# Optimization experiments

Measured on AMD Instinct MI355X. Metric: run time of the kernel, lower is better.

## Reference

```python
import jax, jax.numpy as jnp
import numpy as np

B, T, S, H = 4, 256, 512, 512


def setup_inputs() -> dict:
    key = jax.random.key(0)
    ks = jax.random.split(key, 8)
    scale = 1.0 / np.sqrt(H)
    return {
        "decoder_hidden": jax.random.normal(ks[0], (B, T, H), jnp.float32),
        "encoder_outputs": jax.random.normal(ks[1], (B, S, H), jnp.float32),
        "W1": jax.random.uniform(ks[2], (H, H), jnp.float32, -scale, scale),
        "b1": jax.random.uniform(ks[3], (H,), jnp.float32, -scale, scale),
        "W2": jax.random.uniform(ks[4], (H, H), jnp.float32, -scale, scale),
        "b2": jax.random.uniform(ks[5], (H,), jnp.float32, -scale, scale),
        "V": jax.random.uniform(ks[6], (H,), jnp.float32, -scale, scale),
        "bV": jax.random.uniform(ks[7], (), jnp.float32, -scale, scale),
    }


def reference(decoder_hidden, encoder_outputs, W1, b1, W2, b2, V, bV):
    # Projections: q (B,T,H), k (B,S,H)
    q = jnp.einsum("bth,hd->btd", decoder_hidden, W1.T) + b1
    k = jnp.einsum("bsh,hd->bsd", encoder_outputs, W2.T) + b2
    # Additive scores: tanh over broadcast (B,T,S,H), reduced by V -> (B,T,S)
    e = jnp.tanh(q[:, :, None, :] + k[:, None, :, :])
    score = jnp.einsum("btsh,h->bts", e, V) + bV
    attn = jax.nn.softmax(score, axis=-1)
    # Context: (B,T,S) @ (B,S,H) -> (B,T,H)
    context = jnp.einsum("bts,bsh->bth", attn, encoder_outputs)
    return context
```

## Files before the change

kernel.cpp:

```cpp
#include <hip/hip_runtime.h>

#define B 4
#define T 256
#define S 512
#define H 512
#define BT (B*T)

#define PRESCALE 2.8853900817779268f
#define LOG2E 1.4426950408889634f
#define QCLAMP 15.0f

typedef unsigned short u16;
typedef __attribute__((ext_vector_type(8))) short bf16x8;
typedef __attribute__((ext_vector_type(4))) float f32x4;

#if __has_builtin(__builtin_amdgcn_exp2f)
#define EXP2(x) __builtin_amdgcn_exp2f(x)
#else
#define EXP2(x) exp2f(x)
#endif

__device__ __forceinline__ u16 f2bf(float x) {
    unsigned u = __float_as_uint(x);
    u = u + 0x7FFFu + ((u >> 16) & 1u);
    return (u16)(u >> 16);
}

__device__ __forceinline__ void split8(float4 f0, float4 f1, bf16x8& hi, bf16x8& lo) {
    float x[8] = {f0.x, f0.y, f0.z, f0.w, f1.x, f1.y, f1.z, f1.w};
    #pragma unroll
    for (int i = 0; i < 8; ++i) {
        unsigned u = __float_as_uint(x[i]);
        unsigned h = u & 0xFFFF0000u;
        hi[i] = (short)(h >> 16);
        lo[i] = (short)f2bf(x[i] - __uint_as_float(h));
    }
}

__global__ __launch_bounds__(256) void mfma_proj(
    const float* __restrict__ dh, const float* __restrict__ enc,
    const float* __restrict__ W1, const float* __restrict__ W2,
    const float* __restrict__ b1, const float* __restrict__ b2,
    float* __restrict__ abuf, float* __restrict__ bT4,
    u16* __restrict__ encT_hi, u16* __restrict__ encT_lo)
{
    __shared__ u16 lds[4 * 4096];

    const int tid   = threadIdx.x;
    const int n0    = blockIdx.x * 64;
    const int mTile = blockIdx.y;

    if (mTile >= 48) {
        float (*TTf)[65] = reinterpret_cast<float(*)[65]>(lds);
        const int ty = mTile - 48;
        const int bb = ty >> 3;
        const int st = ty & 7;
        const int c64 = tid & 63;
        const int r4  = tid >> 6;
        #pragma unroll
        for (int rr = 0; rr < 16; ++rr) {
            const int r = rr * 4 + r4;
            TTf[r][c64] = enc[((size_t)(bb * S + st * 64 + r)) * H + n0 + c64];
        }
        __syncthreads();
        const int hr = tid >> 2;
        const int sq = (tid & 3) * 16;
        u16* ehp = encT_hi + ((size_t)(bb * H + n0 + hr)) * S + st * 64 + sq;
        u16* elp = encT_lo + ((size_t)(bb * H + n0 + hr)) * S + st * 64 + sq;
        #pragma unroll
        for (int j4 = 0; j4 < 4; ++j4) {
            ushort4 hv, lv;
            #pragma unroll
            for (int jj = 0; jj < 4; ++jj) {
                float x = TTf[sq + j4 * 4 + jj][hr];
                unsigned u = __float_as_uint(x);
                unsigned hb = u & 0xFFFF0000u;
                u16 hh = (u16)(hb >> 16);
                u16 ll = f2bf(x - __uint_as_float(hb));
                if (jj == 0) { hv.x = hh; lv.x = ll; }
                else if (jj == 1) { hv.y = hh; lv.y = ll; }
                else if (jj == 2) { hv.z = hh; lv.z = ll; }
                else { hv.w = hh; lv.w = ll; }
            }
            *(ushort4*)&ehp[j4 * 4] = hv;
            *(ushort4*)&elp[j4 * 4] = lv;
        }
        return;
    }

    const int lane  = tid & 63;
    const int w     = tid >> 6;
    const int mbase = mTile * 64;
    const bool is_q = (mTile < 16);

    const float* Asrc = is_q ? dh : enc;
    const float* Wsrc = is_q ? W1 : W2;
    const int arow = is_q ? mbase : (mbase - 1024);

    const int wm = (w & 1) * 32;
    const int wn = (w >> 1) * 32;

    const int r0  = tid >> 3;
    const int kc0 = tid & 7;

    f32x4 acc[2][2] = {};

    for (int kb = 0; kb < 8; ++kb) {
        const int k0 = kb * 64 + kc0 * 8;
        const size_t ga0 = (size_t)(arow + r0) * 512 + k0;
        const size_t ga1 = (size_t)(arow + r0 + 32) * 512 + k0;
        const size_t gw0 = (size_t)(n0 + r0) * 512 + k0;
        const size_t gw1 = (size_t)(n0 + r0 + 32) * 512 + k0;
        bf16x8 ah0, al0, ah1, al1, wh0, wl0, wh1, wl1;
        split8(*(const float4*)&Asrc[ga0], *(const float4*)&Asrc[ga0 + 4], ah0, al0);
        split8(*(const float4*)&Asrc[ga1], *(const float4*)&Asrc[ga1 + 4], ah1, al1);
        split8(*(const float4*)&Wsrc[gw0], *(const float4*)&Wsrc[gw0 + 4], wh0, wl0);
        split8(*(const float4*)&Wsrc[gw1], *(const float4*)&Wsrc[gw1 + 4], wh1, wl1);
        __syncthreads();
        const int sw  = (kc0 ^ (r0 & 7)) << 3;
        const int s0o = r0 * 64 + sw;
        const int s1o = (r0 + 32) * 64 + sw;
        *(bf16x8*)&lds[0 * 4096 + s0o] = ah0;  *(bf16x8*)&lds[0 * 4096 + s1o] = ah1;
        *(bf16x8*)&lds[1 * 4096 + s0o] = al0;  *(bf16x8*)&lds[1 * 4096 + s1o] = al1;
        *(bf16x8*)&lds[2 * 4096 + s0o] = wh0;  *(bf16x8*)&lds[2 * 4096 + s1o] = wh1;
        *(bf16x8*)&lds[3 * 4096 + s0o] = wl0;  *(bf16x8*)&lds[3 * 4096 + s1o] = wl1;
        __syncthreads();

        #pragma unroll
        for (int ks = 0; ks < 2; ++ks) {
            const int kg = ks * 4 + (lane >> 4);
            bf16x8 amh[2], aml[2], bnh[2], bnl[2];
            #pragma unroll
            for (int ms = 0; ms < 2; ++ms) {
                const int row = wm + ms * 16 + (lane & 15);
                const int off = row * 64 + ((kg ^ (row & 7)) << 3);
                amh[ms] = *(const bf16x8*)&lds[0 * 4096 + off];
                aml[ms] = *(const bf16x8*)&lds[1 * 4096 + off];
            }
            #pragma unroll
            for (int ns = 0; ns < 2; ++ns) {
                const int row = wn + ns * 16 + (lane & 15);
                const int off = row * 64 + ((kg ^ (row & 7)) << 3);
                bnh[ns] = *(const bf16x8*)&lds[2 * 4096 + off];
                bnl[ns] = *(const bf16x8*)&lds[3 * 4096 + off];
            }
            #pragma unroll
            for (int ms = 0; ms < 2; ++ms)
                #pragma unroll
                for (int ns = 0; ns < 2; ++ns) {
                    acc[ms][ns] = __builtin_amdgcn_mfma_f32_16x16x32_bf16(amh[ms], bnh[ns], acc[ms][ns], 0, 0, 0);
                    acc[ms][ns] = __builtin_amdgcn_mfma_f32_16x16x32_bf16(amh[ms], bnl[ns], acc[ms][ns], 0, 0, 0);
                    acc[ms][ns] = __builtin_amdgcn_mfma_f32_16x16x32_bf16(aml[ms], bnh[ns], acc[ms][ns], 0, 0, 0);
                }
        }
    }

    const float* bias = is_q ? b1 : b2;
    #pragma unroll
    for (int ns = 0; ns < 2; ++ns) {
        const int gn = n0 + wn + ns * 16 + (lane & 15);
        const float bv = bias[gn];
        #pragma unroll
        for (int ms = 0; ms < 2; ++ms) {
            #pragma unroll
            for (int r = 0; r < 4; ++r) {
                const int gm = mbase + wm + ms * 16 + (lane >> 4) * 4 + r;
                const float e = EXP2(fminf((acc[ms][ns][r] + bv) * PRESCALE, QCLAMP));
                if (is_q) {
                    abuf[(size_t)gm * 512 + gn] = e;
                } else {
                    const int srow = gm - 1024;
                    const int bb = srow >> 9, ss = srow & 511;
                    bT4[(((size_t)(bb * 128 + (gn >> 2)) * 512) + ss) * 4 + (gn & 3)] = e;
                }
            }
        }
    }
}

__device__ __forceinline__ float quad_term(float4 qa, float4 kb, float4 v4, float acc) {
    float x0 = fmaf(qa.x, kb.x, 1.f);
    float x1 = fmaf(qa.y, kb.y, 1.f);
    float x2 = fmaf(qa.z, kb.z, 1.f);
    float x3 = fmaf(qa.w, kb.w, 1.f);
    float p01 = x0 * x1, p23 = x2 * x3;
    float n01 = fmaf(v4.y, x0, v4.x * x1);
    float n23 = fmaf(v4.w, x2, v4.z * x3);
    float num = fmaf(n23, p01, n01 * p23);
    float den = p01 * p23;
    return fmaf(num, __builtin_amdgcn_rcpf(den), acc);
}

__global__ __launch_bounds__(512) void score_e(
    const float* __restrict__ abuf, const float* __restrict__ bT4,
    const float* __restrict__ Vp, const float* __restrict__ bVp,
    u16* __restrict__ e_hi, u16* __restrict__ e_lo, float* __restrict__ Zp)
{
    const int tid  = threadIdx.x;
    const int lane = tid & 63;
    const int w    = tid >> 6;
    const int sc   = blockIdx.x;
    const int t0   = blockIdx.y * 16;
    const int b    = blockIdx.z;
    const int s0   = sc * 64;

    float pv = 0.f;
    #pragma unroll
    for (int i = 0; i < 8; ++i) pv += Vp[i * 64 + lane];
    #pragma unroll
    for (int off = 32; off; off >>= 1) pv += __shfl_xor(pv, off);
    pv += bVp[0];

    const int ta = t0 + w * 2;
    const int tb = ta + 1;
    const float* aA = abuf + __builtin_amdgcn_readfirstlane((b * T + ta) * H);
    const float* aB = abuf + __builtin_amdgcn_readfirstlane((b * T + tb) * H);
    const float4* bp = (const float4*)bT4 + (size_t)(b * 128) * S + s0 + lane;

    float accA = 0.f, accB = 0.f;
    #pragma unroll 4
    for (int h4 = 0; h4 < 128; ++h4) {
        float4 kb = bp[(size_t)h4 * S];
        float4 v4 = *(const float4*)&Vp[h4 * 4];
        float4 qA = *(const float4*)&aA[h4 * 4];
        float4 qB = *(const float4*)&aB[h4 * 4];
        accA = quad_term(qA, kb, v4, accA);
        accB = quad_term(qB, kb, v4, accB);
    }
    const float xA = fmaf(-2.f, accA, pv);
    const float xB = fmaf(-2.f, accB, pv);

    const float eA = EXP2(xA * LOG2E);
    const float eB = EXP2(xB * LOG2E);

    float zA = eA, zB = eB;
    #pragma unroll
    for (int off = 32; off; off >>= 1) {
        zA += __shfl_xor(zA, off);
        zB += __shfl_xor(zB, off);
    }

    unsigned uA = __float_as_uint(eA), uB = __float_as_uint(eB);
    unsigned hA = uA & 0xFFFF0000u,   hB = uB & 0xFFFF0000u;
    const size_t rowA = (size_t)(b * T + ta);
    const size_t rowB = (size_t)(b * T + tb);
    e_hi[rowA * S + s0 + lane] = (u16)(hA >> 16);
    e_lo[rowA * S + s0 + lane] = f2bf(eA - __uint_as_float(hA));
    e_hi[rowB * S + s0 + lane] = (u16)(hB >> 16);
    e_lo[rowB * S + s0 + lane] = f2bf(eB - __uint_as_float(hB));

    if (lane == 0) {
        Zp[(size_t)sc * BT + rowA] = zA;
        Zp[(size_t)sc * BT + rowB] = zB;
    }
}

__global__ __launch_bounds__(256) void ctx_mfma(
    const u16* __restrict__ e_hi, const u16* __restrict__ e_lo,
    const u16* __restrict__ eT_hi, const u16* __restrict__ eT_lo,
    const float* __restrict__ Zp, float* __restrict__ out)
{
    __shared__ u16 lds[4 * 4096];
    __shared__ float zinv[64];

    const int tid  = threadIdx.x;
    const int lane = tid & 63;
    const int w    = tid >> 6;
    const int n0   = blockIdx.x * 64;
    const int m0   = blockIdx.y * 64;
    const int b    = blockIdx.z;

    if (tid < 64) {
        float z = 0.f;
        #pragma unroll
        for (int c = 0; c < 8; ++c) z += Zp[(size_t)c * BT + b * T + m0 + tid];
        zinv[tid] = __builtin_amdgcn_rcpf(z);
    }

    const int wm = (w & 1) * 32;
    const int wn = (w >> 1) * 32;
    const int r0  = tid >> 3;
    const int kc0 = tid & 7;

    const size_t abase = (size_t)(b * T + m0);
    const size_t bbase = (size_t)b * H + n0;

    f32x4 acc[2][2] = {};

    for (int kb = 0; kb < 8; ++kb) {
        const int k0 = kb * 64 + kc0 * 8;
        const size_t ga0 = (abase + r0) * S + k0;
        const size_t ga1 = (abase + r0 + 32) * S + k0;
        const size_t gw0 = (bbase + r0) * S + k0;
        const size_t gw1 = (bbase + r0 + 32) * S + k0;
        bf16x8 ah0 = *(const bf16x8*)&e_hi[ga0];
        bf16x8 ah1 = *(const bf16x8*)&e_hi[ga1];
        bf16x8 al0 = *(const bf16x8*)&e_lo[ga0];
        bf16x8 al1 = *(const bf16x8*)&e_lo[ga1];
        bf16x8 wh0 = *(const bf16x8*)&eT_hi[gw0];
        bf16x8 wh1 = *(const bf16x8*)&eT_hi[gw1];
        bf16x8 wl0 = *(const bf16x8*)&eT_lo[gw0];
        bf16x8 wl1 = *(const bf16x8*)&eT_lo[gw1];
        __syncthreads();
        const int sw  = (kc0 ^ (r0 & 7)) << 3;
        const int s0o = r0 * 64 + sw;
        const int s1o = (r0 + 32) * 64 + sw;
        *(bf16x8*)&lds[0 * 4096 + s0o] = ah0;  *(bf16x8*)&lds[0 * 4096 + s1o] = ah1;
        *(bf16x8*)&lds[1 * 4096 + s0o] = al0;  *(bf16x8*)&lds[1 * 4096 + s1o] = al1;
        *(bf16x8*)&lds[2 * 4096 + s0o] = wh0;  *(bf16x8*)&lds[2 * 4096 + s1o] = wh1;
        *(bf16x8*)&lds[3 * 4096 + s0o] = wl0;  *(bf16x8*)&lds[3 * 4096 + s1o] = wl1;
        __syncthreads();

        #pragma unroll
        for (int ks = 0; ks < 2; ++ks) {
            const int kg = ks * 4 + (lane >> 4);
            bf16x8 amh[2], aml[2], bnh[2], bnl[2];
            #pragma unroll
            for (int ms = 0; ms < 2; ++ms) {
                const int row = wm + ms * 16 + (lane & 15);
                const int off = row * 64 + ((kg ^ (row & 7)) << 3);
                amh[ms] = *(const bf16x8*)&lds[0 * 4096 + off];
                aml[ms] = *(const bf16x8*)&lds[1 * 4096 + off];
            }
            #pragma unroll
            for (int ns = 0; ns < 2; ++ns) {
                const int row = wn + ns * 16 + (lane & 15);
                const int off = row * 64 + ((kg ^ (row & 7)) << 3);
                bnh[ns] = *(const bf16x8*)&lds[2 * 4096 + off];
                bnl[ns] = *(const bf16x8*)&lds[3 * 4096 + off];
            }
            #pragma unroll
            for (int ms = 0; ms < 2; ++ms)
                #pragma unroll
                for (int ns = 0; ns < 2; ++ns) {
                    acc[ms][ns] = __builtin_amdgcn_mfma_f32_16x16x32_bf16(amh[ms], bnh[ns], acc[ms][ns], 0, 0, 0);
                    acc[ms][ns] = __builtin_amdgcn_mfma_f32_16x16x32_bf16(amh[ms], bnl[ns], acc[ms][ns], 0, 0, 0);
                    acc[ms][ns] = __builtin_amdgcn_mfma_f32_16x16x32_bf16(aml[ms], bnh[ns], acc[ms][ns], 0, 0, 0);
                }
        }
    }

    #pragma unroll
    for (int ns = 0; ns < 2; ++ns) {
        const int col = n0 + wn + ns * 16 + (lane & 15);
        #pragma unroll
        for (int ms = 0; ms < 2; ++ms) {
            #pragma unroll
            for (int r = 0; r < 4; ++r) {
                const int row = wm + ms * 16 + (lane >> 4) * 4 + r;
                out[((size_t)(b * T + m0 + row)) * H + col] = acc[ms][ns][r] * zinv[row];
            }
        }
    }
}

extern "C" void kernel_launch(void* const* d_in, const int* in_sizes, int n_in,
                              void* d_out, int out_size, void* d_ws, size_t ws_size,
                              hipStream_t stream) {
    const float* dh  = (const float*)d_in[0];
    const float* enc = (const float*)d_in[1];
    const float* W1  = (const float*)d_in[2];
    const float* b1  = (const float*)d_in[3];
    const float* W2  = (const float*)d_in[4];
    const float* b2  = (const float*)d_in[5];
    const float* V   = (const float*)d_in[6];
    const float* bV  = (const float*)d_in[7];

    float* abuf   = (float*)d_ws;
    float* bT4    = abuf + (size_t)B * T * H;
    u16*  encT_hi = (u16*)(bT4 + (size_t)B * S * H);
    u16*  encT_lo = encT_hi + (size_t)B * H * S;
    u16*  e_hi    = encT_lo + (size_t)B * H * S;
    u16*  e_lo    = e_hi + (size_t)B * T * S;
    float* Zp     = (float*)(e_lo + (size_t)B * T * S);

    mfma_proj<<<dim3(8, 80),    dim3(256), 0, stream>>>(dh, enc, W1, W2, b1, b2,
                                                        abuf, bT4, encT_hi, encT_lo);
    score_e  <<<dim3(8, 16, 4), dim3(512), 0, stream>>>(abuf, bT4, V, bV, e_hi, e_lo, Zp);
    ctx_mfma <<<dim3(8, 4, 4),  dim3(256), 0, stream>>>(e_hi, e_lo, encT_hi, encT_lo,
                                                        Zp, (float*)d_out);
}
```

Before: 60.10 us.

## Stage key and query tiles in LDS for score kernel, smaller blocks

The score kernel now loads each 128-wide H chunk of the key tile (64 s positions) and of the query rows into shared memory cooperatively, then computes from LDS instead of reading global memory directly in the inner loop. The block size drops from 512 to 256 threads, with 8 t rows per block and twice as many blocks. This aims to coalesce the global loads and reuse the key tile across warps. In exchange it adds barriers per chunk, 36KB of LDS per block that may limit occupancy, and halves the key reuse per block, so the key tile is read from global twice as often.

```diff
diff --git a/kernel.cpp b/kernel.cpp
--- a/kernel.cpp
+++ b/kernel.cpp
@@ -191,16 +191,19 @@
     return fmaf(num, __builtin_amdgcn_rcpf(den), acc);
 }
 
-__global__ __launch_bounds__(512) void score_e(
+__global__ __launch_bounds__(256) void score_e(
     const float* __restrict__ abuf, const float* __restrict__ bT4,
     const float* __restrict__ Vp, const float* __restrict__ bVp,
     u16* __restrict__ e_hi, u16* __restrict__ e_lo, float* __restrict__ Zp)
 {
+    __shared__ float klds[32 * 64 * 4];
+    __shared__ float qlds[8 * 128];
+
     const int tid  = threadIdx.x;
     const int lane = tid & 63;
     const int w    = tid >> 6;
     const int sc   = blockIdx.x;
-    const int t0   = blockIdx.y * 16;
+    const int t0   = blockIdx.y * 8;
     const int b    = blockIdx.z;
     const int s0   = sc * 64;
 
@@ -213,20 +216,42 @@
 
     const int ta = t0 + w * 2;
     const int tb = ta + 1;
-    const float* aA = abuf + __builtin_amdgcn_readfirstlane((b * T + ta) * H);
-    const float* aB = abuf + __builtin_amdgcn_readfirstlane((b * T + tb) * H);
-    const float4* bp = (const float4*)bT4 + (size_t)(b * 128) * S + s0 + lane;
 
     float accA = 0.f, accB = 0.f;
-    #pragma unroll 4
-    for (int h4 = 0; h4 < 128; ++h4) {
-        float4 kb = bp[(size_t)h4 * S];
-        float4 v4 = *(const float4*)&Vp[h4 * 4];
-        float4 qA = *(const float4*)&aA[h4 * 4];
-        float4 qB = *(const float4*)&aB[h4 * 4];
-        accA = quad_term(qA, kb, v4, accA);
-        accB = quad_term(qB, kb, v4, accB);
-    }
+
+    for (int hc = 0; hc < 4; ++hc) {
+        const int h0 = hc * 128;
+        __syncthreads();
+
+        const float4* kb_src = (const float4*)bT4 + (size_t)(b * 128 + (h0 >> 2)) * S + s0;
+        #pragma unroll
+        for (int j = 0; j < 8; ++j) {
+            const int flat = tid + j * 256;
+            const int i  = flat >> 6;
+            const int si = flat & 63;
+            ((float4*)klds)[flat] = kb_src[(size_t)i * S + si];
+        }
+        {
+            const int row = tid >> 5;
+            const int hh  = (tid & 31) * 4;
+            *(float4*)&qlds[row * 128 + hh] =
+                *(const float4*)&abuf[(size_t)(b * T + t0 + row) * H + h0 + hh];
+        }
+        __syncthreads();
+
+        const float* qA = &qlds[(w * 2 + 0) * 128];
+        const float* qB = &qlds[(w * 2 + 1) * 128];
+        #pragma unroll 8
+        for (int i = 0; i < 32; ++i) {
+            float4 kb = ((const float4*)klds)[i * 64 + lane];
+            float4 v4 = *(const float4*)&Vp[h0 + i * 4];
+            float4 q_A = *(const float4*)&qA[i * 4];
+            float4 q_B = *(const float4*)&qB[i * 4];
+            accA = quad_term(q_A, kb, v4, accA);
+            accB = quad_term(q_B, kb, v4, accB);
+        }
+    }
+
     const float xA = fmaf(-2.f, accA, pv);
     const float xB = fmaf(-2.f, accB, pv);
 
@@ -376,7 +401,7 @@
 
     mfma_proj<<<dim3(8, 80),    dim3(256), 0, stream>>>(dh, enc, W1, W2, b1, b2,
                                                         abuf, bT4, encT_hi, encT_lo);
-    score_e  <<<dim3(8, 16, 4), dim3(512), 0, stream>>>(abuf, bT4, V, bV, e_hi, e_lo, Zp);
+    score_e  <<<dim3(8, 32, 4), dim3(256), 0, stream>>>(abuf, bT4, V, bV, e_hi, e_lo, Zp);
     ctx_mfma <<<dim3(8, 4, 4),  dim3(256), 0, stream>>>(e_hi, e_lo, encT_hi, encT_lo,
                                                         Zp, (float*)d_out);
 }
```

Measured after the change: 62.53 us. 4.1% more time.
